# Optimization experiments

Hardware: AMD Instinct MI355X
Metric: run time of the kernel (lower is better)

The kernel has to match this reference:

```python
import jax, jax.numpy as jnp
import numpy as np

N = 50000      # nodes
E = 800000     # edges per relation
R = 2          # relations
L = 2          # conv layers
D = 128        # hidden / input channels
G = 64         # graphs in batch
C = 8          # num_classes


def setup_inputs() -> dict:
    key = jax.random.key(0)
    ks = jax.random.split(key, 6)
    x = jax.random.normal(ks[0], (N, D), dtype=jnp.float32)
    W = jax.random.normal(ks[1], (L, R, D, D), dtype=jnp.float32) * 0.05
    b = jnp.zeros((L, R, D), dtype=jnp.float32)
    lin_w = jax.random.normal(ks[2], (D, C), dtype=jnp.float32) * 0.05
    lin_b = jnp.zeros((C,), dtype=jnp.float32)
    edge_index = jax.random.randint(ks[3], (R, 2, E), 0, N, dtype=jnp.int32)
    batch = jnp.sort(jax.random.randint(ks[4], (N,), 0, G, dtype=jnp.int32))
    return {"x": x, "W": W, "b": b, "lin_w": lin_w, "lin_b": lin_b,
            "edge_index": edge_index, "batch": batch}


def _gcn_conv(x, src, dst, inv_sqrt_deg, W_r, b_r):
    """PyG GCNConv: symmetric-normalized aggregation with self loops.
    out[i] = sum_{j->i} d_i^-1/2 d_j^-1/2 (x_j W) + d_i^-1 (x_i W) + b
    where d includes the self loop (in-degree + 1)."""
    xw = x @ W_r                                   # [N, D]
    norm = inv_sqrt_deg[src] * inv_sqrt_deg[dst]   # [E]
    agg = jax.ops.segment_sum(xw[src] * norm[:, None], dst, num_segments=N)
    agg = agg + xw * (inv_sqrt_deg * inv_sqrt_deg)[:, None]  # self-loop msg
    return agg + b_r


def reference(x, W, b, lin_w, lin_b, edge_index, batch):
    # Pre-compute per-relation symmetric normalization (same for all layers).
    inv_sqrt_degs = []
    for r in range(R):
        dst = edge_index[r, 1]
        deg = jax.ops.segment_sum(jnp.ones((E,), x.dtype), dst, num_segments=N) + 1.0
        inv_sqrt_degs.append(jax.lax.rsqrt(deg))

    h = x
    for l in range(L):
        out = jnp.zeros((N, D), x.dtype)
        for r in range(R):  # HeteroConv aggr='sum' over relations
            out = out + _gcn_conv(h, edge_index[r, 0], edge_index[r, 1],
                                  inv_sqrt_degs[r], W[l, r], b[l, r])
        h = jax.nn.relu(out) if l < L - 1 else out

    # global_mean_pool over batch ids
    counts = jax.ops.segment_sum(jnp.ones((N,), x.dtype), batch, num_segments=G)
    sums = jax.ops.segment_sum(h, batch, num_segments=G)
    pooled = sums / jnp.maximum(counts, 1.0)[:, None]   # [G, D]
    # dropout(p=0.5) is identity in eval mode; final Linear
    return pooled @ lin_w + lin_b                        # [G, C]
```

## Files before the change

kernel.cpp:

```cpp
#include <hip/hip_runtime.h>
#include <math.h>

#define NN 50000
#define EE 800000
#define RR 2
#define LL 2
#define DD 128
#define GG 64
#define CCLS 8
#define NBUK 196
#define BCAP 4608
#define BCI  12000

typedef unsigned int uint;
typedef unsigned short ushort;
typedef short bf16x8 __attribute__((ext_vector_type(8)));
typedef float f32x4 __attribute__((ext_vector_type(4)));
typedef float f32x2 __attribute__((ext_vector_type(2)));

#define OFF_AGG   ((size_t)0)
#define OFF_WBT   ((size_t)25600000)
#define OFF_ISD   ((size_t)25731072)
#define OFF_RP    ((size_t)26131072)
#define OFF_CI    ((size_t)26733184)
#define OFF_ZERO  ((size_t)36141184)
#define OFF_T     ((size_t)36175808)
#define ZO_GCUR 0
#define ZO_SUM  1600
#define ZO_CNT  34368
#define ZERO_BYTES 34624

static __device__ __forceinline__ ushort f2b(float f) {
  uint u = __float_as_uint(f);
  uint r = (u + 0x7fffu + ((u >> 16) & 1u)) >> 16;
  return (ushort)r;
}
static __device__ __forceinline__ float blo(uint u) { return __uint_as_float(u << 16); }
static __device__ __forceinline__ float bhi(uint u) { return __uint_as_float(u & 0xffff0000u); }

__global__ __launch_bounds__(256) void k_wprep(const float* __restrict__ W,
                                               ushort* __restrict__ WT) {
  int idx = blockIdx.x * 256 + threadIdx.x;
  int lr = idx >> 14;
  int l = lr >> 1, r = lr & 1;
  int rem = idx & 16383;
  int n = rem >> 7, k = rem & 127;
  WT[l * 32768 + n * 256 + r * 128 + k] = f2b(W[lr * 16384 + k * 128 + n]);
}

__global__ __launch_bounds__(256) void k_xq(const float* __restrict__ x,
                                            uint* __restrict__ T) {
  int idx = blockIdx.x * 256 + threadIdx.x;
  if (idx >= (NN + 1) * 32) return;
  int row = idx >> 5, q = idx & 31;
  uint u = 0;
  if (row < NN) {
    float4 a = ((const float4*)x)[(size_t)row * 32 + q];
    u = __builtin_amdgcn_cvt_pk_fp8_f32(a.x, a.y, 0u, false);
    u = __builtin_amdgcn_cvt_pk_fp8_f32(a.z, a.w, u, true);
  }
  T[idx] = u;
}

__global__ __launch_bounds__(256) void k_part(const int* __restrict__ EI,
                                              int* __restrict__ gcur,
                                              uint* __restrict__ bdata) {
  __shared__ int hist[256];
  __shared__ int sbase[256];
  __shared__ int gbase[256];
  __shared__ int lcur[256];
  __shared__ uint stage[4096];
  __shared__ unsigned char bstage[4096];
  const int r = blockIdx.y;
  const int t = threadIdx.x;
  const int e0 = blockIdx.x * 4096;
  const int cnt = min(4096, EE - e0);
  hist[t] = 0;
  lcur[t] = 0;
  __syncthreads();

  int src[16], dst[16];
  bool val[4];
#pragma unroll
  for (int j = 0; j < 4; ++j) {
    int i4 = (j * 256 + t) * 4;
    val[j] = (i4 < cnt);
    if (val[j]) {
      int4 s4 = *(const int4*)(EI + (size_t)r * 2 * EE + e0 + i4);
      int4 d4 = *(const int4*)(EI + (size_t)r * 2 * EE + EE + e0 + i4);
      src[j * 4 + 0] = s4.x; src[j * 4 + 1] = s4.y; src[j * 4 + 2] = s4.z; src[j * 4 + 3] = s4.w;
      dst[j * 4 + 0] = d4.x; dst[j * 4 + 1] = d4.y; dst[j * 4 + 2] = d4.z; dst[j * 4 + 3] = d4.w;
#pragma unroll
      for (int i = 0; i < 4; ++i) atomicAdd(&hist[dst[j * 4 + i] >> 8], 1);
    }
  }
  __syncthreads();
  int hv = hist[t];
  if (t < NBUK && hv > 0)
    gbase[t] = atomicAdd(&gcur[r * NBUK + t], hv);
  else
    gbase[t] = 0;
  sbase[t] = hv;
  __syncthreads();
  for (int off = 1; off < 256; off <<= 1) {
    int u = (t >= off) ? sbase[t - off] : 0;
    __syncthreads();
    sbase[t] += u;
    __syncthreads();
  }
  int incl = sbase[t];
  hist[t] = incl - hv;
  __syncthreads();
#pragma unroll
  for (int j = 0; j < 4; ++j) {
    if (val[j]) {
#pragma unroll
      for (int i = 0; i < 4; ++i) {
        int d = dst[j * 4 + i];
        int b = d >> 8;
        int p = atomicAdd(&lcur[b], 1);
        int pos = hist[b] + p;
        stage[pos] = ((uint)src[j * 4 + i] << 8) | (uint)(d & 255);
        bstage[pos] = (unsigned char)b;
      }
    }
  }
  __syncthreads();
  for (int s = t; s < cnt; s += 256) {
    int b = (int)bstage[s];
    bdata[(size_t)(r * NBUK + b) * BCAP + gbase[b] + (s - hist[b])] = stage[s];
  }
}

__global__ __launch_bounds__(256) void k_csr1(const uint* __restrict__ bdata,
                                              const int* __restrict__ gcur,
                                              float* __restrict__ isd,
                                              int* __restrict__ rps,
                                              int* __restrict__ rpc,
                                              int* __restrict__ degs) {
  __shared__ int lcnt0[256], lcnt1[256], lrp[256];
  const int b = blockIdx.x;
  const int t = threadIdx.x;
  const int cnt0 = gcur[b];
  const int cnt1 = gcur[NBUK + b];
  const uint* bd0 = bdata + (size_t)b * BCAP;
  const uint* bd1 = bdata + (size_t)(NBUK + b) * BCAP;
  lcnt0[t] = 0; lcnt1[t] = 0;
  __syncthreads();
  for (int s = t; s < cnt0; s += 256) atomicAdd(&lcnt0[bd0[s] & 255u], 1);
  for (int s = t; s < cnt1; s += 256) atomicAdd(&lcnt1[bd1[s] & 255u], 1);
  __syncthreads();
  const int deg0 = lcnt0[t];
  const int deg1 = lcnt1[t];
  const int node = b * 256 + t;
  const int valid = (node < NN) ? 1 : 0;
  const int ng0 = valid ? ((deg0 + 8) >> 3) : 0;
  const int ng1 = valid ? ((deg1 + 8) >> 3) : 0;
  const int sz = (ng0 + ng1) << 3;
  lrp[t] = sz;
  __syncthreads();
  for (int off = 1; off < 256; off <<= 1) {
    int u = (t >= off) ? lrp[t - off] : 0;
    __syncthreads();
    lrp[t] += u;
    __syncthreads();
  }
  const int ex = lrp[t] - sz;
  rps[node] = b * BCI + ex;
  rpc[node] = ng0 | (ng1 << 16);
  degs[node] = deg0 | (deg1 << 16);
  if (valid) {
    isd[node] = rsqrtf((float)(deg0 + 1));
    isd[NN + node] = rsqrtf((float)(deg1 + 1));
  }
}

__global__ __launch_bounds__(256) void k_csr2(const uint* __restrict__ bdata,
                                              const int* __restrict__ gcur,
                                              const float* __restrict__ isd,
                                              const int* __restrict__ rps,
                                              const int* __restrict__ rpc,
                                              const int* __restrict__ degs,
                                              int* __restrict__ ci) {
  __shared__ int lex[256], lb1[256], lcurA[256], lcurB[256];
  __shared__ int cstage[BCI];
  __shared__ int shtot;
  const int b = blockIdx.x;
  const int t = threadIdx.x;
  const int node = b * 256 + t;
  const int cnt0 = gcur[b];
  const int cnt1 = gcur[NBUK + b];
  const uint* bd0 = bdata + (size_t)b * BCAP;
  const uint* bd1 = bdata + (size_t)(NBUK + b) * BCAP;
  const int ex = rps[node] - b * BCI;
  const int meta = rpc[node];
  const int ng0 = meta & 0xffff, ng1 = (meta >> 16) & 0xffff;
  const int dg = degs[node];
  const int deg0 = dg & 0xffff, deg1 = (dg >> 16) & 0xffff;
  lex[t] = ex;
  lb1[t] = ng0 << 3;
  lcurA[t] = 0;
  lcurB[t] = 0;
  if (t == 255) shtot = ex + ((ng0 + ng1) << 3);
  __syncthreads();
  const int tot = shtot;
  if (t < 32) cstage[tot + t] = NN;
  if (node < NN) {
    cstage[ex + deg0] = node | ((uint)f2b(isd[node]) << 16);
    for (int p = deg0 + 1; p < (ng0 << 3); ++p) cstage[ex + p] = NN;
    const int e1 = ex + (ng0 << 3);
    cstage[e1 + deg1] = node | ((uint)f2b(isd[NN + node]) << 16);
    for (int p = deg1 + 1; p < (ng1 << 3); ++p) cstage[e1 + p] = NN;
  }
  for (int s = t; s < cnt0; s += 256) {
    uint pr = bd0[s];
    int j = (int)(pr & 255u);
    int sr = (int)(pr >> 8);
    int p = atomicAdd(&lcurA[j], 1);
    cstage[lex[j] + p] = sr | ((uint)f2b(isd[sr]) << 16);
  }
  for (int s = t; s < cnt1; s += 256) {
    uint pr = bd1[s];
    int j = (int)(pr & 255u);
    int sr = (int)(pr >> 8);
    int p = atomicAdd(&lcurB[j], 1);
    cstage[lex[j] + lb1[j] + p] = sr | ((uint)f2b(isd[NN + sr]) << 16);
  }
  __syncthreads();
  int* co = ci + (size_t)b * BCI;
  const int on = tot + 32;
  for (int s = t; s < on; s += 256) co[s] = cstage[s];
}

#define AGG_STEP(A)                                                            \
  {                                                                            \
    uint e2 = (uint)ce[ip];                                                    \
    int s2 = (ip < lim) ? (int)(e2 & 0xffffu) : NN;                            \
    float f2 = bhi(e2);                                                        \
    ip += 8;                                                                   \
    uint4 d2 = *(const uint4*)(Tb + ((((size_t)(uint)s2) << 7) + cb));         \
    f32x2 sc; sc[0] = f0; sc[1] = f0;                                          \
    f32x2 v;                                                                   \
    v = __builtin_amdgcn_cvt_pk_f32_fp8(d0.x, false); A[0] += v * sc;          \
    v = __builtin_amdgcn_cvt_pk_f32_fp8(d0.x, true);  A[1] += v * sc;          \
    v = __builtin_amdgcn_cvt_pk_f32_fp8(d0.y, false); A[2] += v * sc;          \
    v = __builtin_amdgcn_cvt_pk_f32_fp8(d0.y, true);  A[3] += v * sc;          \
    v = __builtin_amdgcn_cvt_pk_f32_fp8(d0.z, false); A[4] += v * sc;          \
    v = __builtin_amdgcn_cvt_pk_f32_fp8(d0.z, true);  A[5] += v * sc;          \
    v = __builtin_amdgcn_cvt_pk_f32_fp8(d0.w, false); A[6] += v * sc;          \
    v = __builtin_amdgcn_cvt_pk_f32_fp8(d0.w, true);  A[7] += v * sc;          \
    d0 = d1; d1 = d2; f0 = f1; f1 = f2;                                        \
  }

__global__ __launch_bounds__(256, 6) void k_agg(const char* __restrict__ Tb,
                                                const int* __restrict__ rps,
                                                const int* __restrict__ rpc,
                                                const int* __restrict__ ci,
                                                const float* __restrict__ isd,
                                                ushort* __restrict__ aggo) {
  const int w = threadIdx.x >> 6;
  const int lane = threadIdx.x & 63;
  const int g = lane >> 3, c = lane & 7;
  const int node = blockIdx.x * 4 + w;
  const size_t cb = (size_t)c * 16;

  const int meta = rpc[node];
  const int ng0 = meta & 0xffff;
  const int ng1 = (meta >> 16) & 0xffff;
  const int lim = (ng0 + ng1) << 3;
  const int* ce = ci + rps[node];
  const int nsafe = (node < NN) ? node : 0;
  const float di0 = isd[nsafe];
  const float di1 = isd[NN + nsafe];

  int ip = g;
  uint e0 = (uint)ce[ip];
  int s0 = (ip < lim) ? (int)(e0 & 0xffffu) : NN;
  float f0 = bhi(e0);
  ip += 8;
  uint4 d0 = *(const uint4*)(Tb + ((((size_t)(uint)s0) << 7) + cb));
  uint e1 = (uint)ce[ip];
  int s1 = (ip < lim) ? (int)(e1 & 0xffffu) : NN;
  float f1 = bhi(e1);
  ip += 8;
  uint4 d1 = *(const uint4*)(Tb + ((((size_t)(uint)s1) << 7) + cb));

  f32x2 a0[8], a1[8];
#pragma unroll
  for (int j = 0; j < 8; ++j) { a0[j][0] = 0.f; a0[j][1] = 0.f; a1[j][0] = 0.f; a1[j][1] = 0.f; }

  for (int q = 0; q < ng0; ++q) AGG_STEP(a0);
  for (int q = 0; q < ng1; ++q) AGG_STEP(a1);

#pragma unroll
  for (int mask = 8; mask <= 32; mask <<= 1) {
#pragma unroll
    for (int j = 0; j < 8; ++j) {
      f32x2 o, p;
      o[0] = __shfl_xor(a0[j][0], mask);
      o[1] = __shfl_xor(a0[j][1], mask);
      p[0] = __shfl_xor(a1[j][0], mask);
      p[1] = __shfl_xor(a1[j][1], mask);
      a0[j] += o;
      a1[j] += p;
    }
  }

  if (g == 0 && node < NN) {
    ushort* row = aggo + (size_t)node * 256;
    uint pk[8];
#pragma unroll
    for (int j = 0; j < 4; ++j) {
      pk[2 * j] = (uint)f2b(a0[2 * j][0] * di0) | ((uint)f2b(a0[2 * j][1] * di0) << 16);
      pk[2 * j + 1] = (uint)f2b(a0[2 * j + 1][0] * di0) | ((uint)f2b(a0[2 * j + 1][1] * di0) << 16);
    }
    *(uint4*)(row + c * 16) = make_uint4(pk[0], pk[1], pk[2], pk[3]);
    *(uint4*)(row + c * 16 + 8) = make_uint4(pk[4], pk[5], pk[6], pk[7]);
#pragma unroll
    for (int j = 0; j < 4; ++j) {
      pk[2 * j] = (uint)f2b(a1[2 * j][0] * di1) | ((uint)f2b(a1[2 * j][1] * di1) << 16);
      pk[2 * j + 1] = (uint)f2b(a1[2 * j + 1][0] * di1) | ((uint)f2b(a1[2 * j + 1][1] * di1) << 16);
    }
    *(uint4*)(row + 128 + c * 16) = make_uint4(pk[0], pk[1], pk[2], pk[3]);
    *(uint4*)(row + 128 + c * 16 + 8) = make_uint4(pk[4], pk[5], pk[6], pk[7]);
  }
}

#define AL_S 72
#define WT_S 72
template <int OUT>
__global__ __launch_bounds__(256) void k_gemm(const ushort* __restrict__ A,
                                              const ushort* __restrict__ WTg,
                                              const float* __restrict__ bias,
                                              uint* __restrict__ Yfp8,
                                              ushort* __restrict__ Ybf) {
  __shared__ ushort WTl[128 * WT_S];
  __shared__ ushort Al[64 * AL_S];
  const int m0b = blockIdx.x * 64;
  const int t = threadIdx.x;
  const int w = t >> 6, L = t & 63, q = L >> 4, ln = L & 15;

  f32x4 acc[8];
#pragma unroll
  for (int nt = 0; nt < 8; ++nt) {
    acc[nt][0] = 0.f; acc[nt][1] = 0.f; acc[nt][2] = 0.f; acc[nt][3] = 0.f;
  }

  for (int hh = 0; hh < 4; ++hh) {
    __syncthreads();
    {
      int n = t >> 1, half = t & 1;
#pragma unroll
      for (int j = 0; j < 4; ++j)
        *(uint4*)(&WTl[n * WT_S + half * 32 + j * 8]) =
            *(const uint4*)(WTg + n * 256 + hh * 64 + half * 32 + j * 8);
      int row = t >> 2, seg = t & 3;
      int gm = m0b + row;
      if (gm < NN) {
#pragma unroll
        for (int j = 0; j < 2; ++j)
          *(uint4*)(&Al[row * AL_S + seg * 16 + j * 8]) =
              *(const uint4*)(A + (size_t)gm * 256 + hh * 64 + seg * 16 + j * 8);
      } else {
        uint4 z = make_uint4(0, 0, 0, 0);
#pragma unroll
        for (int j = 0; j < 2; ++j) *(uint4*)(&Al[row * AL_S + seg * 16 + j * 8]) = z;
      }
    }
    __syncthreads();
#pragma unroll
    for (int kk = 0; kk < 2; ++kk) {
      bf16x8 bfr = *(const bf16x8*)(&Al[(w * 16 + ln) * AL_S + kk * 32 + q * 8]);
#pragma unroll
      for (int nt = 0; nt < 8; ++nt) {
        bf16x8 a = *(const bf16x8*)(&WTl[(nt * 16 + ln) * WT_S + kk * 32 + q * 8]);
        acc[nt] = __builtin_amdgcn_mfma_f32_16x16x32_bf16(a, bfr, acc[nt], 0, 0, 0);
      }
    }
  }
  const int m = m0b + w * 16 + ln;
  if (OUT == 0) {
    if (m < NN) {
      uint* yp = Yfp8 + (size_t)m * 32;
#pragma unroll
      for (int nt = 0; nt < 8; ++nt) {
        int n0 = nt * 16 + q * 4;
        float4 bL = *(const float4*)(bias + n0);
        float4 bH = *(const float4*)(bias + 128 + n0);
        f32x4 v = acc[nt];
        float o0 = fmaxf(v[0] + bL.x + bH.x, 0.f);
        float o1 = fmaxf(v[1] + bL.y + bH.y, 0.f);
        float o2 = fmaxf(v[2] + bL.z + bH.z, 0.f);
        float o3 = fmaxf(v[3] + bL.w + bH.w, 0.f);
        uint u = __builtin_amdgcn_cvt_pk_fp8_f32(o0, o1, 0u, false);
        u = __builtin_amdgcn_cvt_pk_fp8_f32(o2, o3, u, true);
        yp[nt * 4 + q] = u;
      }
    } else if (m == NN) {
      uint* yp = Yfp8 + (size_t)m * 32;
#pragma unroll
      for (int nt = 0; nt < 8; ++nt) yp[nt * 4 + q] = 0u;
    }
  } else {
    if (m < NN) {
      uint* yp = (uint*)(Ybf + (size_t)m * 256);
#pragma unroll
      for (int nt = 0; nt < 8; ++nt) {
        int n0 = nt * 16 + q * 4;
        float4 bL = *(const float4*)(bias + n0);
        float4 bH = *(const float4*)(bias + 128 + n0);
        f32x4 v = acc[nt];
        float o0 = v[0] + bL.x + bH.x;
        float o1 = v[1] + bL.y + bH.y;
        float o2 = v[2] + bL.z + bH.z;
        float o3 = v[3] + bL.w + bH.w;
        yp[nt * 8 + q * 2] = (uint)f2b(o0) | ((uint)f2b(o1) << 16);
        yp[nt * 8 + q * 2 + 1] = (uint)f2b(o2) | ((uint)f2b(o3) << 16);
      }
    }
  }
}

#define PCHUNK 32
__global__ __launch_bounds__(64) void k_pool(const uint* __restrict__ h,
                                             const int* __restrict__ batch,
                                             float* __restrict__ sums,
                                             int* __restrict__ counts) {
  int lane = threadIdx.x;
  int n0 = blockIdx.x * PCHUNK;
  int n1 = n0 + PCHUNK;
  if (n1 > NN) n1 = NN;
  if (n0 >= NN) return;
  float aLo = 0.f, aHi = 0.f;
  int cnt = 0;
  int g = batch[n0];
  uint u = h[(size_t)n0 * 128 + lane];
  for (int n = n0; n < n1; ++n) {
    uint unext = 0;
    int gnext = g;
    if (n + 1 < n1) {
      unext = h[(size_t)(n + 1) * 128 + lane];
      gnext = batch[n + 1];
    }
    aLo += blo(u);
    aHi += bhi(u);
    cnt++;
    if (n + 1 < n1 && gnext != g) {
      atomicAdd(&sums[g * DD + lane * 2], aLo);
      atomicAdd(&sums[g * DD + lane * 2 + 1], aHi);
      if (lane == 0) atomicAdd(&counts[g], cnt);
      aLo = 0.f; aHi = 0.f; cnt = 0;
      g = gnext;
    }
    u = unext;
  }
  atomicAdd(&sums[g * DD + lane * 2], aLo);
  atomicAdd(&sums[g * DD + lane * 2 + 1], aHi);
  if (lane == 0) atomicAdd(&counts[g], cnt);
}

__global__ __launch_bounds__(512) void k_final(const float* __restrict__ sums,
                                               const int* __restrict__ counts,
                                               const float* __restrict__ lin_w,
                                               const float* __restrict__ lin_b,
                                               float* __restrict__ out) {
  int t = threadIdx.x;
  int g = t >> 3, co = t & 7;
  float cnt = (float)counts[g];
  if (cnt < 1.f) cnt = 1.f;
  float inv = 1.f / cnt;
  float v = lin_b[co];
  for (int d = 0; d < DD; ++d) v += (sums[g * DD + d] * inv) * lin_w[d * CCLS + co];
  out[t] = v;
}

extern "C" void kernel_launch(void* const* d_in, const int* in_sizes, int n_in,
                              void* d_out, int out_size, void* d_ws, size_t ws_size,
                              hipStream_t stream) {
  (void)in_sizes; (void)n_in; (void)out_size; (void)ws_size;
  const float* x     = (const float*)d_in[0];
  const float* W     = (const float*)d_in[1];
  const float* b     = (const float*)d_in[2];
  const float* lin_w = (const float*)d_in[3];
  const float* lin_b = (const float*)d_in[4];
  const int*   EI    = (const int*)d_in[5];
  const int*   batch = (const int*)d_in[6];
  float* out = (float*)d_out;

  char* ws = (char*)d_ws;
  ushort* agg   = (ushort*)(ws + OFF_AGG);
  uint*   bdata = (uint*)(ws + OFF_AGG);
  ushort* Ws    = (ushort*)(ws + OFF_WBT);
  float*  isd   = (float*)(ws + OFF_ISD);
  int*    rps   = (int*)(ws + OFF_RP);
  int*    rpc   = rps + NBUK * 256;
  int*    degs  = rpc + NBUK * 256;
  int*    ci    = (int*)(ws + OFF_CI);
  uint*   T     = (uint*)(ws + OFF_T);
  char*   zb    = ws + OFF_ZERO;
  int*    gcur  = (int*)(zb + ZO_GCUR);
  float*  sums  = (float*)(zb + ZO_SUM);
  int*    counts= (int*)(zb + ZO_CNT);

  (void)hipMemsetAsync(zb, 0, ZERO_BYTES, stream);

  k_wprep<<<256, 256, 0, stream>>>(W, Ws);
  k_xq<<<((NN + 1) * 32 + 255) / 256, 256, 0, stream>>>(x, T);
  k_part<<<dim3((EE + 4095) / 4096, RR), 256, 0, stream>>>(EI, gcur, bdata);
  k_csr1<<<NBUK, 256, 0, stream>>>(bdata, gcur, isd, rps, rpc, degs);
  k_csr2<<<NBUK, 256, 0, stream>>>(bdata, gcur, isd, rps, rpc, degs, ci);

  const int gagg = NBUK * 256 / 4;
  const int ggemm = (NN + 63) / 64;
  k_agg<<<gagg, 256, 0, stream>>>((const char*)T, rps, rpc, ci, isd, agg);
  k_gemm<0><<<ggemm, 256, 0, stream>>>(agg, Ws, b, T, nullptr);
  k_agg<<<gagg, 256, 0, stream>>>((const char*)T, rps, rpc, ci, isd, agg);
  k_gemm<1><<<ggemm, 256, 0, stream>>>(agg, Ws + 32768, b + 256, nullptr, agg);

  k_pool<<<(NN + PCHUNK - 1) / PCHUNK, 64, 0, stream>>>((const uint*)agg, batch, sums, counts);
  k_final<<<1, GG * CCLS, 0, stream>>>(sums, counts, lin_w, lin_b, out);
}
```

Baseline: 297.5 us.

## Fold destination norm into edge weights, deepen gather prefetch, reuse one accumulator

The CSR build now stores the full symmetric weight d_src^-1/2 * d_dst^-1/2 (and d^-1 for the self loop) per edge, caching destination norms in shared memory, so the aggregation kernel no longer loads isd or scales at write-out. The aggregation kernel keeps a single accumulator set reused for both relations, reducing and writing each half separately. It also deepens the software-pipelined prefetch from two to three rows in flight and drops the occupancy hint from launch_bounds. Folding the product before bf16 rounding slightly changes numerics, and the extra prefetch adds registers that may lower occupancy.

```diff
diff --git a/kernel.cpp b/kernel.cpp
--- a/kernel.cpp
+++ b/kernel.cpp
@@ -183,6 +183,7 @@
                                               const int* __restrict__ degs,
                                               int* __restrict__ ci) {
   __shared__ int lex[256], lb1[256], lcurA[256], lcurB[256];
+  __shared__ float lisd0[256], lisd1[256];
   __shared__ int cstage[BCI];
   __shared__ int shtot;
   const int b = blockIdx.x;
@@ -197,19 +198,23 @@
   const int ng0 = meta & 0xffff, ng1 = (meta >> 16) & 0xffff;
   const int dg = degs[node];
   const int deg0 = dg & 0xffff, deg1 = (dg >> 16) & 0xffff;
+  const int valid = (node < NN) ? 1 : 0;
   lex[t] = ex;
   lb1[t] = ng0 << 3;
   lcurA[t] = 0;
   lcurB[t] = 0;
+  lisd0[t] = valid ? isd[node] : 0.f;
+  lisd1[t] = valid ? isd[NN + node] : 0.f;
   if (t == 255) shtot = ex + ((ng0 + ng1) << 3);
   __syncthreads();
   const int tot = shtot;
   if (t < 32) cstage[tot + t] = NN;
-  if (node < NN) {
-    cstage[ex + deg0] = node | ((uint)f2b(isd[node]) << 16);
+  if (valid) {
+    const float d0 = lisd0[t], d1 = lisd1[t];
+    cstage[ex + deg0] = node | ((uint)f2b(d0 * d0) << 16);
     for (int p = deg0 + 1; p < (ng0 << 3); ++p) cstage[ex + p] = NN;
     const int e1 = ex + (ng0 << 3);
-    cstage[e1 + deg1] = node | ((uint)f2b(isd[NN + node]) << 16);
+    cstage[e1 + deg1] = node | ((uint)f2b(d1 * d1) << 16);
     for (int p = deg1 + 1; p < (ng1 << 3); ++p) cstage[e1 + p] = NN;
   }
   for (int s = t; s < cnt0; s += 256) {
@@ -217,14 +222,14 @@
     int j = (int)(pr & 255u);
     int sr = (int)(pr >> 8);
     int p = atomicAdd(&lcurA[j], 1);
-    cstage[lex[j] + p] = sr | ((uint)f2b(isd[sr]) << 16);
+    cstage[lex[j] + p] = sr | ((uint)f2b(isd[sr] * lisd0[j]) << 16);
   }
   for (int s = t; s < cnt1; s += 256) {
     uint pr = bd1[s];
     int j = (int)(pr & 255u);
     int sr = (int)(pr >> 8);
     int p = atomicAdd(&lcurB[j], 1);
-    cstage[lex[j] + lb1[j] + p] = sr | ((uint)f2b(isd[NN + sr]) << 16);
+    cstage[lex[j] + lb1[j] + p] = sr | ((uint)f2b(isd[NN + sr] * lisd1[j]) << 16);
   }
   __syncthreads();
   int* co = ci + (size_t)b * BCI;
@@ -232,32 +237,54 @@
   for (int s = t; s < on; s += 256) co[s] = cstage[s];
 }
 
-#define AGG_STEP(A)                                                            \
+#define AGG_STEP()                                                             \
   {                                                                            \
-    uint e2 = (uint)ce[ip];                                                    \
-    int s2 = (ip < lim) ? (int)(e2 & 0xffffu) : NN;                            \
-    float f2 = bhi(e2);                                                        \
+    uint e3 = (uint)ce[ip];                                                    \
+    int s3 = (ip < lim) ? (int)(e3 & 0xffffu) : NN;                            \
+    float f3 = bhi(e3);                                                        \
     ip += 8;                                                                   \
-    uint4 d2 = *(const uint4*)(Tb + ((((size_t)(uint)s2) << 7) + cb));         \
+    uint4 d3 = *(const uint4*)(Tb + ((((size_t)(uint)s3) << 7) + cb));         \
     f32x2 sc; sc[0] = f0; sc[1] = f0;                                          \
     f32x2 v;                                                                   \
-    v = __builtin_amdgcn_cvt_pk_f32_fp8(d0.x, false); A[0] += v * sc;          \
-    v = __builtin_amdgcn_cvt_pk_f32_fp8(d0.x, true);  A[1] += v * sc;          \
-    v = __builtin_amdgcn_cvt_pk_f32_fp8(d0.y, false); A[2] += v * sc;          \
-    v = __builtin_amdgcn_cvt_pk_f32_fp8(d0.y, true);  A[3] += v * sc;          \
-    v = __builtin_amdgcn_cvt_pk_f32_fp8(d0.z, false); A[4] += v * sc;          \
-    v = __builtin_amdgcn_cvt_pk_f32_fp8(d0.z, true);  A[5] += v * sc;          \
-    v = __builtin_amdgcn_cvt_pk_f32_fp8(d0.w, false); A[6] += v * sc;          \
-    v = __builtin_amdgcn_cvt_pk_f32_fp8(d0.w, true);  A[7] += v * sc;          \
-    d0 = d1; d1 = d2; f0 = f1; f1 = f2;                                        \
-  }
-
-__global__ __launch_bounds__(256, 6) void k_agg(const char* __restrict__ Tb,
-                                                const int* __restrict__ rps,
-                                                const int* __restrict__ rpc,
-                                                const int* __restrict__ ci,
-                                                const float* __restrict__ isd,
-                                                ushort* __restrict__ aggo) {
+    v = __builtin_amdgcn_cvt_pk_f32_fp8(d0.x, false); acc[0] += v * sc;        \
+    v = __builtin_amdgcn_cvt_pk_f32_fp8(d0.x, true);  acc[1] += v * sc;        \
+    v = __builtin_amdgcn_cvt_pk_f32_fp8(d0.y, false); acc[2] += v * sc;        \
+    v = __builtin_amdgcn_cvt_pk_f32_fp8(d0.y, true);  acc[3] += v * sc;        \
+    v = __builtin_amdgcn_cvt_pk_f32_fp8(d0.z, false); acc[4] += v * sc;        \
+    v = __builtin_amdgcn_cvt_pk_f32_fp8(d0.z, true);  acc[5] += v * sc;        \
+    v = __builtin_amdgcn_cvt_pk_f32_fp8(d0.w, false); acc[6] += v * sc;        \
+    v = __builtin_amdgcn_cvt_pk_f32_fp8(d0.w, true);  acc[7] += v * sc;        \
+    d0 = d1; d1 = d2; d2 = d3; f0 = f1; f1 = f2; f2 = f3;                      \
+  }
+
+#define AGG_REDUCE_WRITE(halfoff)                                              \
+  {                                                                            \
+    _Pragma("unroll")                                                          \
+    for (int mask = 8; mask <= 32; mask <<= 1) {                               \
+      _Pragma("unroll")                                                        \
+      for (int j = 0; j < 8; ++j) {                                            \
+        f32x2 o;                                                               \
+        o[0] = __shfl_xor(acc[j][0], mask);                                    \
+        o[1] = __shfl_xor(acc[j][1], mask);                                    \
+        acc[j] += o;                                                           \
+      }                                                                        \
+    }                                                                          \
+    if (g == 0 && node < NN) {                                                 \
+      ushort* row = aggo + (size_t)node * 256 + (halfoff);                     \
+      uint pk[8];                                                              \
+      _Pragma("unroll")                                                        \
+      for (int j = 0; j < 8; ++j)                                              \
+        pk[j] = (uint)f2b(acc[j][0]) | ((uint)f2b(acc[j][1]) << 16);           \
+      *(uint4*)(row + c * 16) = make_uint4(pk[0], pk[1], pk[2], pk[3]);        \
+      *(uint4*)(row + c * 16 + 8) = make_uint4(pk[4], pk[5], pk[6], pk[7]);    \
+    }                                                                          \
+  }
+
+__global__ __launch_bounds__(256) void k_agg(const char* __restrict__ Tb,
+                                             const int* __restrict__ rps,
+                                             const int* __restrict__ rpc,
+                                             const int* __restrict__ ci,
+                                             ushort* __restrict__ aggo) {
   const int w = threadIdx.x >> 6;
   const int lane = threadIdx.x & 63;
   const int g = lane >> 3, c = lane & 7;
@@ -269,9 +296,6 @@
   const int ng1 = (meta >> 16) & 0xffff;
   const int lim = (ng0 + ng1) << 3;
   const int* ce = ci + rps[node];
-  const int nsafe = (node < NN) ? node : 0;
-  const float di0 = isd[nsafe];
-  const float di1 = isd[NN + nsafe];
 
   int ip = g;
   uint e0 = (uint)ce[ip];
@@ -284,46 +308,22 @@
   float f1 = bhi(e1);
   ip += 8;
   uint4 d1 = *(const uint4*)(Tb + ((((size_t)(uint)s1) << 7) + cb));
-
-  f32x2 a0[8], a1[8];
-#pragma unroll
-  for (int j = 0; j < 8; ++j) { a0[j][0] = 0.f; a0[j][1] = 0.f; a1[j][0] = 0.f; a1[j][1] = 0.f; }
-
-  for (int q = 0; q < ng0; ++q) AGG_STEP(a0);
-  for (int q = 0; q < ng1; ++q) AGG_STEP(a1);
-
-#pragma unroll
-  for (int mask = 8; mask <= 32; mask <<= 1) {
-#pragma unroll
-    for (int j = 0; j < 8; ++j) {
-      f32x2 o, p;
-      o[0] = __shfl_xor(a0[j][0], mask);
-      o[1] = __shfl_xor(a0[j][1], mask);
-      p[0] = __shfl_xor(a1[j][0], mask);
-      p[1] = __shfl_xor(a1[j][1], mask);
-      a0[j] += o;
-      a1[j] += p;
-    }
-  }
-
-  if (g == 0 && node < NN) {
-    ushort* row = aggo + (size_t)node * 256;
-    uint pk[8];
-#pragma unroll
-    for (int j = 0; j < 4; ++j) {
-      pk[2 * j] = (uint)f2b(a0[2 * j][0] * di0) | ((uint)f2b(a0[2 * j][1] * di0) << 16);
-      pk[2 * j + 1] = (uint)f2b(a0[2 * j + 1][0] * di0) | ((uint)f2b(a0[2 * j + 1][1] * di0) << 16);
-    }
-    *(uint4*)(row + c * 16) = make_uint4(pk[0], pk[1], pk[2], pk[3]);
-    *(uint4*)(row + c * 16 + 8) = make_uint4(pk[4], pk[5], pk[6], pk[7]);
-#pragma unroll
-    for (int j = 0; j < 4; ++j) {
-      pk[2 * j] = (uint)f2b(a1[2 * j][0] * di1) | ((uint)f2b(a1[2 * j][1] * di1) << 16);
-      pk[2 * j + 1] = (uint)f2b(a1[2 * j + 1][0] * di1) | ((uint)f2b(a1[2 * j + 1][1] * di1) << 16);
-    }
-    *(uint4*)(row + 128 + c * 16) = make_uint4(pk[0], pk[1], pk[2], pk[3]);
-    *(uint4*)(row + 128 + c * 16 + 8) = make_uint4(pk[4], pk[5], pk[6], pk[7]);
-  }
+  uint e2 = (uint)ce[ip];
+  int s2 = (ip < lim) ? (int)(e2 & 0xffffu) : NN;
+  float f2 = bhi(e2);
+  ip += 8;
+  uint4 d2 = *(const uint4*)(Tb + ((((size_t)(uint)s2) << 7) + cb));
+
+  f32x2 acc[8];
+#pragma unroll
+  for (int j = 0; j < 8; ++j) { acc[j][0] = 0.f; acc[j][1] = 0.f; }
+
+  for (int q = 0; q < ng0; ++q) AGG_STEP();
+  AGG_REDUCE_WRITE(0);
+#pragma unroll
+  for (int j = 0; j < 8; ++j) { acc[j][0] = 0.f; acc[j][1] = 0.f; }
+  for (int q = 0; q < ng1; ++q) AGG_STEP();
+  AGG_REDUCE_WRITE(128);
 }
 
 #define AL_S 72
@@ -512,9 +512,9 @@
 
   const int gagg = NBUK * 256 / 4;
   const int ggemm = (NN + 63) / 64;
-  k_agg<<<gagg, 256, 0, stream>>>((const char*)T, rps, rpc, ci, isd, agg);
+  k_agg<<<gagg, 256, 0, stream>>>((const char*)T, rps, rpc, ci, agg);
   k_gemm<0><<<ggemm, 256, 0, stream>>>(agg, Ws, b, T, nullptr);
-  k_agg<<<gagg, 256, 0, stream>>>((const char*)T, rps, rpc, ci, isd, agg);
+  k_agg<<<gagg, 256, 0, stream>>>((const char*)T, rps, rpc, ci, agg);
   k_gemm<1><<<ggemm, 256, 0, stream>>>(agg, Ws + 32768, b + 256, nullptr, agg);
 
   k_pool<<<(NN + PCHUNK - 1) / PCHUNK, 64, 0, stream>>>((const uint*)agg, batch, sums, counts);
```

After: 299.1 us. About the same (+0.5%).
